# Optimization experiments

Measured on AMD Instinct MI355X. Metric: run time of the kernel, lower is better.

The kernel has to match this reference:

```python
import jax, jax.numpy as jnp
import numpy as np

NEG = -10000.0
MAX_SPAN_LEN = 30
TOP_LAMBDA = 0.4
NUM_CATS = 7
FFNN = 1024
HID = 1024
B, S = 2, 2048
MAX_K = int(S * TOP_LAMBDA)  # 819; static top-k size (input_masks are full)


def fc(x, W, b, g, beta):
    # FullyConnectedLayer: Linear -> GELU(exact) -> LayerNorm (dropout = identity in eval)
    h = jax.nn.gelu(x @ W.T + b, approximate=False)
    mu = jnp.mean(h, axis=-1, keepdims=True)
    var = jnp.var(h, axis=-1, keepdims=True)
    return (h - mu) / jnp.sqrt(var + 1e-5) * g + beta


def setup_inputs():
    key = jax.random.key(0)
    ks = iter(jax.random.split(key, 48))
    def rn(shape, scale=0.02):
        return jax.random.normal(next(ks), shape, jnp.float32) * scale
    NF = NUM_CATS * FFNN
    inp = {
        'input_emb': jax.random.normal(next(ks), (B, S, HID), jnp.float32),
        'input_masks': jnp.ones((B, S), jnp.int32),
        # start/end mention MLPs
        'sm_W': rn((FFNN, HID)), 'sm_b': jnp.zeros((FFNN,)), 'sm_g': jnp.ones((FFNN,)), 'sm_beta': jnp.zeros((FFNN,)),
        'em_W': rn((FFNN, HID)), 'em_b': jnp.zeros((FFNN,)), 'em_g': jnp.ones((FFNN,)), 'em_beta': jnp.zeros((FFNN,)),
        # mention start/end classifiers (Linear(F,1)) and s2e classifier
        'ms_w': rn((FFNN,)), 'ms_b': jnp.zeros(()),
        'me_w': rn((FFNN,)), 'me_b': jnp.zeros(()),
        's2e_W': rn((FFNN, FFNN)), 's2e_b': jnp.zeros((FFNN,)),
        # coref start/end all-category MLPs (output num_cats*ffnn)
        'cs_W': rn((NF, HID)), 'cs_b': jnp.zeros((NF,)), 'cs_g': jnp.ones((NF,)), 'cs_beta': jnp.zeros((NF,)),
        'ce_W': rn((NF, HID)), 'ce_b': jnp.zeros((NF,)), 'ce_g': jnp.ones((NF,)), 'ce_beta': jnp.zeros((NF,)),
        # per-category bilinear antecedent weights/biases
        'Ws2s': rn((NUM_CATS, FFNN, FFNN)), 'We2e': rn((NUM_CATS, FFNN, FFNN)),
        'Ws2e': rn((NUM_CATS, FFNN, FFNN)), 'We2s': rn((NUM_CATS, FFNN, FFNN)),
        'Bs2s': rn((NUM_CATS, FFNN)), 'Be2e': rn((NUM_CATS, FFNN)),
        'Bs2e': rn((NUM_CATS, FFNN)), 'Be2s': rn((NUM_CATS, FFNN)),
    }
    return inp


def reference(input_emb, input_masks, sm_W, sm_b, sm_g, sm_beta, em_W, em_b, em_g, em_beta,
              ms_w, ms_b, me_w, me_b, s2e_W, s2e_b, cs_W, cs_b, cs_g, cs_beta,
              ce_W, ce_b, ce_g, ce_beta, Ws2s, We2e, Ws2e, We2s, Bs2s, Be2e, Bs2e, Be2s):
    # --- mention scores ---
    s = fc(input_emb, sm_W, sm_b, sm_g, sm_beta)   # [B,S,F]
    e = fc(input_emb, em_W, em_b, em_g, em_beta)   # [B,S,F]
    sm = s @ ms_w + ms_b                            # [B,S]
    em = e @ me_w + me_b                            # [B,S]
    joint = jnp.einsum('bsf,btf->bst', s @ s2e_W.T + s2e_b, e)
    scores = joint + sm[:, :, None] + em[:, None, :]
    i = jnp.arange(S)
    band = ((i[None, :] >= i[:, None]) & (i[None, :] - i[:, None] < MAX_SPAN_LEN)).astype(scores.dtype)
    scores = scores + (1.0 - band) * NEG            # mask_tensor (additive)
    # --- top-k span pruning ---
    flat = scores.reshape(B, S * S)
    _, idx = jax.lax.top_k(flat, MAX_K)
    k = (jnp.sum(input_masks, axis=-1).astype(jnp.float32) * TOP_LAMBDA).astype(jnp.int32)
    span_mask = (jnp.arange(MAX_K)[None, :] < k[:, None]).astype(jnp.int32)  # [B,K]
    idx = idx * span_mask + (1 - span_mask) * (S * S - 1)
    idx = jnp.sort(idx, axis=-1)
    start_ids = idx // S
    end_ids = idx % S
    topk_scores = jnp.take_along_axis(flat, idx, axis=1)          # [B,K]
    pair_scores = topk_scores[:, :, None] + topk_scores[:, None, :]
    # --- per-category coref reps (gather then MLP) ---
    start_reps = jnp.take_along_axis(input_emb, start_ids[:, :, None], axis=1)  # [B,K,H]
    end_reps = jnp.take_along_axis(input_emb, end_ids[:, :, None], axis=1)
    a_s = fc(start_reps, cs_W, cs_b, cs_g, cs_beta).reshape(B, MAX_K, NUM_CATS, FFNN).transpose(0, 2, 1, 3)
    a_e = fc(end_reps, ce_W, ce_b, ce_g, ce_beta).reshape(B, MAX_K, NUM_CATS, FFNN).transpose(0, 2, 1, 3)
    # --- per-category bilinear antecedent scores ---
    def bil(x, W, y):
        return jnp.einsum('bnkf,nfg,bnlg->bnkl', x, W, y)
    logits = bil(a_s, Ws2s, a_s) + bil(a_e, We2e, a_e) + bil(a_s, Ws2e, a_e) + bil(a_e, We2s, a_s)
    biases = (jnp.einsum('bnkf,nf->bnk', a_s, Bs2s) + jnp.einsum('bnkf,nf->bnk', a_e, Be2e)
              + jnp.einsum('bnkf,nf->bnk', a_e, Bs2e) + jnp.einsum('bnkf,nf->bnk', a_s, Be2s))[:, :, None, :]
    coref = logits + biases                                        # [B,N,K,K]
    kk = jnp.arange(MAX_K)
    tril = (kk[None, :] < kk[:, None]).astype(coref.dtype)         # strictly-lower (diag=-1)
    mask = tril[None, None] * span_mask[:, None, None, :].astype(coref.dtype)
    coref = coref + (1.0 - mask) * NEG
    return coref + pair_scores[:, None]
```

## Files before the change

### kernel.cpp

```cpp
#include <hip/hip_runtime.h>
#include <hip/hip_bf16.h>
#include <math.h>

#define S_    2048
#define NC_   7
#define MAXK  819
#define NK    1024
#define KP    896
#define Z_    14
#define NEGV  (-10000.0f)

typedef __attribute__((ext_vector_type(8))) short bf16x8;
typedef __attribute__((ext_vector_type(4))) float f32x4;

#define CFENCE asm volatile("" ::: "memory")
#define BAR    do { CFENCE; __builtin_amdgcn_s_barrier(); CFENCE; } while (0)

__device__ __forceinline__ void gload_lds16(const void* g, void* l) {
  __builtin_amdgcn_global_load_lds((const __attribute__((address_space(1))) unsigned int*)g,
                                   (__attribute__((address_space(3))) unsigned int*)l, 16, 0, 0);
}

__device__ __forceinline__ float gelu_exact(float x) {
  return 0.5f * x * (1.0f + erff(x * 0.70710678118654752f));
}
__device__ __forceinline__ unsigned short f2bf(float x) {
  __hip_bfloat16 h = __float2bfloat16(x);
  return *(unsigned short*)&h;
}
__device__ __forceinline__ float bf2f(unsigned short u) {
  __hip_bfloat16 h; *(unsigned short*)&h = u;
  return __bfloat162float(h);
}
__device__ __forceinline__ unsigned fkey(float f) {
  unsigned u = __float_as_uint(f);
  return (u & 0x80000000u) ? ~u : (u | 0x80000000u);
}

template<bool OBF16, int EPI>
__global__ __launch_bounds__(512, 2) void k_gemm8(
    const __hip_bfloat16* __restrict__ A, const __hip_bfloat16* __restrict__ B,
    void* __restrict__ Cv, const float* __restrict__ bias1, const float* __restrict__ bias2,
    const float* __restrict__ tkv, const int* __restrict__ kvp,
    int K, int nbn, long strideA, long strideB, int bmod7, long strideC,
    int ldc, int Mstore, int Nstore)
{
  __shared__ __align__(16) char lds[2][65536];
  const int tid = threadIdx.x;
  const int z = blockIdx.z;
  const int nwg = gridDim.x;
  const int xcd = blockIdx.x & 7, loc = blockIdx.x >> 3;
  const int q = nwg >> 3, r = nwg & 7;
  const int wg = (xcd < r ? xcd * (q + 1) : r * (q + 1) + (xcd - r) * q) + loc;
  const int bm = wg / nbn, bn = wg % nbn;
  const int m0 = bm * 256, n0 = bn * 256;
  const __hip_bfloat16* pA = A + (long)z * strideA;
  const __hip_bfloat16* pB = B + (long)(bmod7 ? (z % 7) : z) * strideB;
  const int wave = tid >> 6, lane = tid & 63;
  const int wm = wave >> 2, wn = wave & 3;
  const int lr = lane & 15, kh = lane >> 4;
  const long Kb = (long)K * 2;

  f32x4 acc[8][4];
  #pragma unroll
  for (int i = 0; i < 8; ++i)
    #pragma unroll
    for (int j = 0; j < 4; ++j)
      #pragma unroll
      for (int rr = 0; rr < 4; ++rr) acc[i][j][rr] = 0.0f;

  auto stageHalf = [&](int bb, int isB, int rh, int kt) {
    const long kbyte = (long)kt * 128;
    const char* basep = isB ? (const char*)pB + (long)(n0 + rh * 128) * Kb
                            : (const char*)pA + (long)(m0 + rh * 128) * Kb;
    #pragma unroll
    for (int j = 0; j < 2; ++j) {
      int off = j * 8192 + tid * 16;
      int row = off >> 7, col = off & 127;
      int gc = col ^ (((rh * 128 + row) & 7) << 4);
      gload_lds16(basep + (long)row * Kb + kbyte + gc,
                  &lds[bb][isB * 32768 + (rh * 128 + row) * 128 + col]);
    }
  };
  auto readA = [&](int c, int g, int kk) -> bf16x8 {
    int row = wm * 128 + g * 16 + lr;
    int colb = kk * 64 + kh * 16;
    return *(const bf16x8*)&lds[c][row * 128 + (colb ^ ((row & 7) << 4))];
  };
  auto readB = [&](int c, int ni, int kk) -> bf16x8 {
    int row = wn * 64 + ni * 16 + lr;
    int colb = kk * 64 + kh * 16;
    return *(const bf16x8*)&lds[c][32768 + row * 128 + (colb ^ ((row & 7) << 4))];
  };
  auto mfma4 = [&](int g0, bf16x8* af, bf16x8* bfr) {
    __builtin_amdgcn_s_setprio(1);
    #pragma unroll
    for (int mi = 0; mi < 4; ++mi)
      #pragma unroll
      for (int ni = 0; ni < 4; ++ni)
        acc[g0 + mi][ni] = __builtin_amdgcn_mfma_f32_16x16x32_bf16(af[mi], bfr[ni], acc[g0 + mi][ni], 0, 0, 0);
    __builtin_amdgcn_s_setprio(0);
  };

  const int nt = K >> 6;
  stageHalf(0, 1, 0, 0);
  stageHalf(0, 1, 1, 0);
  stageHalf(0, 0, 0, 0);
  stageHalf(0, 0, 1, 0);
  if (nt > 1) { stageHalf(1, 1, 0, 1); asm volatile("s_waitcnt vmcnt(2)" ::: "memory"); }
  else        { asm volatile("s_waitcnt vmcnt(0)" ::: "memory"); }
  BAR;

  bf16x8 bfr[4], a0f[4], a1f[4];
  for (int t = 0; t < nt; ++t) {
    const int c = t & 1, cn = c ^ 1;
    #pragma unroll
    for (int i = 0; i < 4; ++i) bfr[i] = readB(c, i, 0);
    #pragma unroll
    for (int i = 0; i < 4; ++i) a0f[i] = readA(c, i, 0);
    if (t + 1 < nt) stageHalf(cn, 1, 1, t + 1);
    BAR;
    mfma4(0, a0f, bfr);
    BAR;
    #pragma unroll
    for (int i = 0; i < 4; ++i) a1f[i] = readA(c, 4 + i, 0);
    if (t + 1 < nt) stageHalf(cn, 0, 0, t + 1);
    BAR;
    mfma4(4, a1f, bfr);
    BAR;
    #pragma unroll
    for (int i = 0; i < 4; ++i) bfr[i] = readB(c, i, 1);
    #pragma unroll
    for (int i = 0; i < 4; ++i) a0f[i] = readA(c, i, 1);
    if (t + 1 < nt) stageHalf(cn, 0, 1, t + 1);
    BAR;
    mfma4(0, a0f, bfr);
    BAR;
    #pragma unroll
    for (int i = 0; i < 4; ++i) a1f[i] = readA(c, 4 + i, 1);
    if (t + 2 < nt) { stageHalf(c, 1, 0, t + 2); asm volatile("s_waitcnt vmcnt(2)" ::: "memory"); }
    else            { asm volatile("s_waitcnt vmcnt(0)" ::: "memory"); }
    BAR;
    mfma4(4, a1f, bfr);
    BAR;
  }

  const long coff = (long)z * strideC;
  int kval = 0, bb_ = 0;
  if (EPI == 2) { bb_ = z / NC_; kval = kvp[bb_]; }
  #pragma unroll
  for (int mi = 0; mi < 8; ++mi) {
    #pragma unroll
    for (int ni = 0; ni < 4; ++ni) {
      int n = n0 + wn * 64 + ni * 16 + lr;
      if (n >= Nstore) continue;
      float badd = 0.f;
      if (EPI == 0) { if (bias1) badd = bias1[n]; }
      if (EPI == 1) badd = (n >= 1024) ? bias2[n - 1024] : bias1[n];
      if (EPI == 2) badd = bias1[z * NK + n] + tkv[bb_ * NK + n];
      #pragma unroll
      for (int rr = 0; rr < 4; ++rr) {
        int m = m0 + wm * 128 + mi * 16 + kh * 4 + rr;
        if (m >= Mstore) continue;
        float v = acc[mi][ni][rr] + badd;
        if (EPI == 2) {
          v += tkv[bb_ * NK + m];
          if (!(n < m && n < kval)) v += NEGV;
        }
        if (OBF16) ((__hip_bfloat16*)Cv)[coff + (long)m * ldc + n] = __float2bfloat16(v);
        else       ((float*)Cv)[coff + (long)m * ldc + n] = v;
      }
    }
  }
}

template<int EPI, int BN>
__global__ __launch_bounds__(512, 1) void k_gemm44(
    const __hip_bfloat16* __restrict__ A, const __hip_bfloat16* __restrict__ B,
    float* __restrict__ Cv, const float* __restrict__ bias1, const float* __restrict__ bias2,
    int K, int nbn, int ldc, int Mstore, int Nstore)
{
  constexpr int NI = BN / 64;
  constexpr int NBH = BN / 128;
  __shared__ __align__(16) char lds[3][16384 + BN * 128];
  const int tid = threadIdx.x;
  const int nwg = gridDim.x;
  const int xcd = blockIdx.x & 7, loc = blockIdx.x >> 3;
  const int q = nwg >> 3, r = nwg & 7;
  const int wg = (xcd < r ? xcd * (q + 1) : r * (q + 1) + (xcd - r) * q) + loc;
  const int bm = wg / nbn, bn = wg % nbn;
  const int m0 = bm * 128, n0 = bn * BN;
  const int wave = tid >> 6, lane = tid & 63;
  const int wm = wave >> 2, wn = wave & 3;
  const int lr = lane & 15, kh = lane >> 4;
  const long Kb = (long)K * 2;

  f32x4 acc[4][NI];
  #pragma unroll
  for (int i = 0; i < 4; ++i)
    #pragma unroll
    for (int j = 0; j < NI; ++j)
      #pragma unroll
      for (int rr = 0; rr < 4; ++rr) acc[i][j][rr] = 0.0f;

  auto stageA = [&](int bb, int kt) {
    const long kbyte = (long)kt * 128;
    const char* basep = (const char*)A + (long)m0 * Kb;
    #pragma unroll
    for (int j = 0; j < 2; ++j) {
      int off = j * 8192 + tid * 16;
      int row = off >> 7, col = off & 127;
      int gc = col ^ ((row & 7) << 4);
      gload_lds16(basep + (long)row * Kb + kbyte + gc, &lds[bb][row * 128 + col]);
    }
  };
  auto stageB = [&](int bb, int kt, int rh) {
    const long kbyte = (long)kt * 128;
    const char* basep = (const char*)B + (long)(n0 + rh * 128) * Kb;
    #pragma unroll
    for (int j = 0; j < 2; ++j) {
      int off = j * 8192 + tid * 16;
      int row = off >> 7, col = off & 127;
      int gc = col ^ (((rh * 128 + row) & 7) << 4);
      gload_lds16(basep + (long)row * Kb + kbyte + gc,
                  &lds[bb][16384 + (rh * 128 + row) * 128 + col]);
    }
  };
  auto readA = [&](int c, int g, int kk) -> bf16x8 {
    int row = wm * 64 + g * 16 + lr;
    int colb = kk * 64 + kh * 16;
    return *(const bf16x8*)&lds[c][row * 128 + (colb ^ ((row & 7) << 4))];
  };
  auto readB = [&](int c, int ni, int kk) -> bf16x8 {
    int row = wn * (NI * 16) + ni * 16 + lr;
    int colb = kk * 64 + kh * 16;
    return *(const bf16x8*)&lds[c][16384 + row * 128 + (colb ^ ((row & 7) << 4))];
  };
  auto mfmaAll = [&](bf16x8* af, bf16x8* bfr) {
    __builtin_amdgcn_s_setprio(1);
    #pragma unroll
    for (int mi = 0; mi < 4; ++mi)
      #pragma unroll
      for (int ni = 0; ni < NI; ++ni)
        acc[mi][ni] = __builtin_amdgcn_mfma_f32_16x16x32_bf16(af[mi], bfr[ni], acc[mi][ni], 0, 0, 0);
    __builtin_amdgcn_s_setprio(0);
  };

  const int nt = K >> 6;
  stageA(0, 0);
  #pragma unroll
  for (int rh = 0; rh < NBH; ++rh) stageB(0, 0, rh);
  if (nt > 1) {
    stageA(1, 1);
    #pragma unroll
    for (int rh = 0; rh < NBH; ++rh) stageB(1, 1, rh);
    if (BN == 256) asm volatile("s_waitcnt vmcnt(6)" ::: "memory");
    else           asm volatile("s_waitcnt vmcnt(4)" ::: "memory");
  } else {
    asm volatile("s_waitcnt vmcnt(0)" ::: "memory");
  }
  BAR;

  bf16x8 af[4], bfr[NI];
  int ct = 0;
  for (int t = 0; t < nt; ++t) {
    const int b2 = (ct + 2 >= 3) ? ct - 1 : ct + 2;
    #pragma unroll
    for (int i = 0; i < NI; ++i) bfr[i] = readB(ct, i, 0);
    #pragma unroll
    for (int i = 0; i < 4; ++i) af[i] = readA(ct, i, 0);
    if (t + 2 < nt) stageA(b2, t + 2);
    BAR;
    mfmaAll(af, bfr);
    BAR;
    #pragma unroll
    for (int i = 0; i < NI; ++i) bfr[i] = readB(ct, i, 1);
    #pragma unroll
    for (int i = 0; i < 4; ++i) af[i] = readA(ct, i, 1);
    if (t + 2 < nt) {
      #pragma unroll
      for (int rh = 0; rh < NBH; ++rh) stageB(b2, t + 2, rh);
      if (BN == 256) asm volatile("s_waitcnt vmcnt(6)" ::: "memory");
      else           asm volatile("s_waitcnt vmcnt(4)" ::: "memory");
    } else {
      asm volatile("s_waitcnt vmcnt(0)" ::: "memory");
    }
    BAR;
    mfmaAll(af, bfr);
    BAR;
    ct = (ct + 1 >= 3) ? 0 : ct + 1;
  }

  #pragma unroll
  for (int mi = 0; mi < 4; ++mi) {
    #pragma unroll
    for (int ni = 0; ni < NI; ++ni) {
      int n = n0 + wn * (NI * 16) + ni * 16 + lr;
      if (n >= Nstore) continue;
      float badd = 0.f;
      if (EPI == 0) { if (bias1) badd = bias1[n]; }
      if (EPI == 1) badd = (n >= 1024) ? bias2[n - 1024] : bias1[n];
      #pragma unroll
      for (int rr = 0; rr < 4; ++rr) {
        int m = m0 + wm * 64 + mi * 16 + kh * 4 + rr;
        if (m >= Mstore) continue;
        Cv[(long)m * ldc + n] = acc[mi][ni][rr] + badd;
      }
    }
  }
}

template<bool APAT>
__global__ __launch_bounds__(256) void k_packsplit3(const float* __restrict__ s1, long stride1,
                                                    const float* __restrict__ s2, int split,
                                                    __hip_bfloat16* __restrict__ dst) {
  long idx4 = ((long)blockIdx.x * 256 + threadIdx.x) * 4;
  int rrow = (int)(idx4 >> 10), c = (int)(idx4 & 1023);
  const float* src = (rrow < split) ? s1 + (long)rrow * stride1 + c
                                    : s2 + (long)(rrow - split) * 1024 + c;
  float4 v = *(const float4*)src;
  float f[4] = {v.x, v.y, v.z, v.w};
  unsigned short h[4], l4[4];
  #pragma unroll
  for (int i = 0; i < 4; ++i) {
    h[i] = f2bf(f[i]);
    l4[i] = f2bf(f[i] - bf2f(h[i]));
  }
  unsigned short* d = (unsigned short*)dst + (long)rrow * 3072;
  ushort4 hv = {h[0], h[1], h[2], h[3]};
  ushort4 lv = {l4[0], l4[1], l4[2], l4[3]};
  *(ushort4*)(d + c)        = hv;
  *(ushort4*)(d + 1024 + c) = APAT ? hv : lv;
  *(ushort4*)(d + 2048 + c) = APAT ? lv : hv;
}

__global__ __launch_bounds__(256) void k_cast4(const float* __restrict__ x,
                                               __hip_bfloat16* __restrict__ y, long n4) {
  long i = (long)blockIdx.x * 256 + threadIdx.x;
  if (i >= n4) return;
  float4 v = ((const float4*)x)[i];
  ushort4 o = {f2bf(v.x), f2bf(v.y), f2bf(v.z), f2bf(v.w)};
  ((ushort4*)y)[i] = o;
}

__global__ __launch_bounds__(256) void k_packBbig(const float* __restrict__ Ws2s,
                                                  const float* __restrict__ We2e,
                                                  const float* __restrict__ Ws2e,
                                                  const float* __restrict__ We2s,
                                                  __hip_bfloat16* __restrict__ dst) {
  long idx4 = ((long)blockIdx.x * 256 + threadIdx.x) * 4;
  long rowid = idx4 >> 11;
  int c = (int)(idx4 & 2047);
  int cat = (int)(rowid >> 11);
  int n = (int)(rowid & 2047);
  const float* src;
  if (n < 1024) src = (c < 1024) ? Ws2s + ((long)cat * 1024 + n) * 1024 + c
                                 : Ws2e + ((long)cat * 1024 + n) * 1024 + (c - 1024);
  else          src = (c < 1024) ? We2s + ((long)cat * 1024 + (n - 1024)) * 1024 + c
                                 : We2e + ((long)cat * 1024 + (n - 1024)) * 1024 + (c - 1024);
  float4 v = *(const float4*)src;
  ushort4 o = {f2bf(v.x), f2bf(v.y), f2bf(v.z), f2bf(v.w)};
  *(ushort4*)((unsigned short*)dst + idx4) = o;
}

__global__ __launch_bounds__(512) void k_ln_se(float* __restrict__ se,
                                               const float* __restrict__ sg, const float* __restrict__ sbe,
                                               const float* __restrict__ eg, const float* __restrict__ ebe,
                                               const float* __restrict__ msw, const float* __restrict__ msb,
                                               const float* __restrict__ mew, const float* __restrict__ meb,
                                               float* __restrict__ smv, float* __restrict__ emv,
                                               __hip_bfloat16* __restrict__ ssp) {
  int r = blockIdx.x;
  int tid = threadIdx.x;
  int half = tid >> 8;
  int c4 = tid & 255;
  int w8 = tid >> 6;
  const float* g    = half ? eg : sg;
  const float* beta = half ? ebe : sbe;
  const float* wv   = half ? mew : msw;
  float4* rowp = (float4*)(se + (long)r * 2048 + half * 1024);
  float4 x = rowp[c4];
  float v[4] = {gelu_exact(x.x), gelu_exact(x.y), gelu_exact(x.z), gelu_exact(x.w)};
  float s = v[0] + v[1] + v[2] + v[3];
  float s2 = v[0]*v[0] + v[1]*v[1] + v[2]*v[2] + v[3]*v[3];
  __shared__ float red0[8], red1[8];
  for (int off = 32; off; off >>= 1) { s += __shfl_xor(s, off); s2 += __shfl_xor(s2, off); }
  if ((tid & 63) == 0) { red0[w8] = s; red1[w8] = s2; }
  __syncthreads();
  s  = red0[half*4] + red0[half*4+1] + red0[half*4+2] + red0[half*4+3];
  s2 = red1[half*4] + red1[half*4+1] + red1[half*4+2] + red1[half*4+3];
  float mu  = s / 1024.0f;
  float var = s2 / 1024.0f - mu * mu;
  float inv = 1.0f / sqrtf(var + 1e-5f);
  float4 gg = ((const float4*)g)[c4], bb = ((const float4*)beta)[c4];
  float y[4] = {(v[0]-mu)*inv*gg.x + bb.x, (v[1]-mu)*inv*gg.y + bb.y,
                (v[2]-mu)*inv*gg.z + bb.z, (v[3]-mu)*inv*gg.w + bb.w};
  float4 w4 = ((const float4*)wv)[c4];
  float d = y[0]*w4.x + y[1]*w4.y + y[2]*w4.z + y[3]*w4.w;
  for (int off = 32; off; off >>= 1) d += __shfl_xor(d, off);
  __syncthreads();
  if ((tid & 63) == 0) red0[w8] = d;
  __syncthreads();
  if ((tid & 255) == 0) {
    float dv = red0[half*4] + red0[half*4+1] + red0[half*4+2] + red0[half*4+3];
    if (half == 0) smv[r] = dv + msb[0];
    else           emv[r] = dv + meb[0];
  }
  if (half == 0) {
    unsigned short h[4], l4[4];
    #pragma unroll
    for (int i = 0; i < 4; ++i) { h[i] = f2bf(y[i]); l4[i] = f2bf(y[i] - bf2f(h[i])); }
    ushort4 hv = {h[0], h[1], h[2], h[3]};
    ushort4 lv = {l4[0], l4[1], l4[2], l4[3]};
    unsigned short* dst = (unsigned short*)ssp + (long)r * 3072 + c4 * 4;
    *(ushort4*)dst          = hv;
    *(ushort4*)(dst + 1024) = hv;
    *(ushort4*)(dst + 2048) = lv;
  } else {
    float4 yo = {y[0], y[1], y[2], y[3]};
    rowp[c4] = yo;
  }
}

__global__ __launch_bounds__(256) void k_gelu_ln_cats(const __hip_bfloat16* __restrict__ h,
                                                      const float* __restrict__ g,
                                                      const float* __restrict__ beta,
                                                      __hip_bfloat16* __restrict__ a_cat, int half) {
  int r = blockIdx.x;
  int b = (r >= KP) ? 1 : 0, k = r - KP * b;
  const ushort4* row = (const ushort4*)((const unsigned short*)h + (long)r * 7168);
  float v[28];
  float s = 0.f, s2 = 0.f;
  #pragma unroll
  for (int j = 0; j < 7; ++j) {
    ushort4 u = row[threadIdx.x + 256 * j];
    #pragma unroll
    for (int e = 0; e < 4; ++e) {
      float x = bf2f(((const unsigned short*)&u)[e]);
      float ge = gelu_exact(x);
      v[j * 4 + e] = ge; s += ge; s2 += ge * ge;
    }
  }
  __shared__ float red0[4], red1[4];
  for (int off = 32; off; off >>= 1) { s += __shfl_xor(s, off); s2 += __shfl_xor(s2, off); }
  int w = threadIdx.x >> 6;
  if ((threadIdx.x & 63) == 0) { red0[w] = s; red1[w] = s2; }
  __syncthreads();
  s  = red0[0] + red0[1] + red0[2] + red0[3];
  s2 = red1[0] + red1[1] + red1[2] + red1[3];
  float mu  = s / 7168.0f;
  float var = s2 / 7168.0f - mu * mu;
  float inv = 1.0f / sqrtf(var + 1e-5f);
  #pragma unroll
  for (int j = 0; j < 7; ++j) {
    int c0 = (threadIdx.x + 256 * j) * 4;
    int n = c0 >> 10, f = c0 & 1023;
    unsigned short o[4];
    #pragma unroll
    for (int e = 0; e < 4; ++e)
      o[e] = f2bf((v[j * 4 + e] - mu) * inv * g[c0 + e] + beta[c0 + e]);
    ushort4 ov = {o[0], o[1], o[2], o[3]};
    *(ushort4*)((unsigned short*)a_cat + ((long)((b * NC_ + n) * NK + k)) * 2048 + half * 1024 + f) = ov;
  }
}

__global__ __launch_bounds__(512) void k_band(const float* __restrict__ s2m,
                                              const float* __restrict__ se,
                                              const float* __restrict__ smv,
                                              const float* __restrict__ emv,
                                              float* __restrict__ band) {
  __shared__ float ebuf[2][1024];
  int blk = blockIdx.x;
  int b = blk >> 8;
  int s0 = (blk & 255) * 8;
  int w = threadIdx.x >> 6, l = threadIdx.x & 63;
  int s = s0 + w;
  int tid = threadIdx.x;
  float sreg[16];
  const float* sp = s2m + ((long)(b << 11) + s) * 1024;
  #pragma unroll
  for (int qq = 0; qq < 16; ++qq) sreg[qq] = sp[l + 64 * qq];
  float myS = smv[(b << 11) + s];
  if (l < 32) {
    int j = l;
    if (j >= 30 || s + j >= S_)
      band[((long)(b << 11) + s) * 32 + j] = -3.0e38f;
  }
  {
    const float* ep = se + ((long)(b << 11) + s0) * 2048 + 1024;
    ebuf[0][tid * 2]     = ep[tid * 2];
    ebuf[0][tid * 2 + 1] = ep[tid * 2 + 1];
  }
  for (int it = 0; it < 37; ++it) {
    int t = s0 + it;
    __syncthreads();
    if (it + 1 < 37 && s0 + it + 1 < S_) {
      const float* ep = se + ((long)(b << 11) + s0 + it + 1) * 2048 + 1024;
      ebuf[(it + 1) & 1][tid * 2]     = ep[tid * 2];
      ebuf[(it + 1) & 1][tid * 2 + 1] = ep[tid * 2 + 1];
    }
    int j = t - s;
    if (t < S_ && j >= 0 && j < 30) {
      const float* eb = ebuf[it & 1];
      float acc = 0.f;
      #pragma unroll
      for (int qq = 0; qq < 16; ++qq) acc += sreg[qq] * eb[l + 64 * qq];
      for (int off = 32; off; off >>= 1) acc += __shfl_xor(acc, off);
      if (l == 0)
        band[((long)(b << 11) + s) * 32 + j] = acc + myS + emv[(b << 11) + t];
    }
  }
}

__global__ __launch_bounds__(1024) void k_tkzero(unsigned* __restrict__ ghist,
                                                 unsigned* __restrict__ gcnt) {
  int i = blockIdx.x * 1024 + threadIdx.x;
  if (i < 2 * 4096) ghist[i] = 0;
  if (i < 2) gcnt[i] = 0;
}

__global__ __launch_bounds__(1024) void k_tkhist(const float* __restrict__ band,
                                                 unsigned* __restrict__ ghist) {
  int b = blockIdx.y;
  const float* bb = band + (long)b * 65536;
  __shared__ unsigned lh[4096];
  int tid = threadIdx.x;
  #pragma unroll
  for (int j = 0; j < 4; ++j) lh[tid + j * 1024] = 0;
  __syncthreads();
  int base = blockIdx.x * 4096;
  #pragma unroll
  for (int j = 0; j < 4; ++j) {
    unsigned key = fkey(bb[base + tid + j * 1024]);
    atomicAdd(&lh[key >> 20], 1u);
  }
  __syncthreads();
  #pragma unroll
  for (int j = 0; j < 4; ++j) {
    unsigned v = lh[tid + j * 1024];
    if (v) atomicAdd(&ghist[b * 4096 + tid + j * 1024], v);
  }
}

__global__ __launch_bounds__(1024) void k_tkscan(const unsigned* __restrict__ ghist,
                                                 const int* __restrict__ masks,
                                                 unsigned* __restrict__ sel) {
  int b = blockIdx.x;
  int tid = threadIdx.x;
  __shared__ unsigned cs[1024];
  __shared__ int red[16];
  __shared__ int sh_kv;
  int pm = masks[b * S_ + tid] + masks[b * S_ + 1024 + tid];
  for (int off = 32; off; off >>= 1) pm += __shfl_xor(pm, off);
  if ((tid & 63) == 0) red[tid >> 6] = pm;
  __syncthreads();
  if (tid == 0) {
    int msum = 0;
    for (int i = 0; i < 16; ++i) msum += red[i];
    int kv = (int)((float)msum * 0.4f);
    if (kv > MAXK) kv = MAXK;
    sh_kv = kv;
  }
  __syncthreads();
  int kv = sh_kv;
  unsigned hbin[4];
  unsigned ssum = 0;
  #pragma unroll
  for (int j = 0; j < 4; ++j) { hbin[j] = ghist[b * 4096 + tid * 4 + j]; ssum += hbin[j]; }
  cs[tid] = ssum;
  __syncthreads();
  for (int off = 1; off < 1024; off <<= 1) {
    unsigned add = (tid + off < 1024) ? cs[tid + off] : 0u;
    __syncthreads();
    cs[tid] += add;
    __syncthreads();
  }
  unsigned above = cs[tid] - ssum;
  if (kv > 0) {
    unsigned aa = above;
    for (int j = 3; j >= 0; --j) {
      if (aa < (unsigned)kv && aa + hbin[j] >= (unsigned)kv) sel[b * 2] = (unsigned)(tid * 4 + j);
      aa += hbin[j];
    }
  }
  if (tid == 0) {
    sel[b * 2 + 1] = (unsigned)kv;
    if (kv == 0) sel[b * 2] = 0xFFFFFFFFu;
  }
}

__global__ __launch_bounds__(1024) void k_tkcollect(const float* __restrict__ band,
                                                    const unsigned* __restrict__ sel,
                                                    unsigned* __restrict__ cand,
                                                    unsigned* __restrict__ gcnt) {
  int b = blockIdx.y;
  const float* bb = band + (long)b * 65536;
  unsigned thr = sel[b * 2];
  int base = blockIdx.x * 4096;
  int tid = threadIdx.x;
  #pragma unroll
  for (int j = 0; j < 4; ++j) {
    int i = base + tid + j * 1024;
    unsigned key = fkey(bb[i]);
    if ((key >> 20) >= thr) {
      unsigned p = atomicAdd(&gcnt[b], 1u);
      cand[(long)b * 65536 + p] = (unsigned)i;
    }
  }
}

__device__ __forceinline__ void bitonic1024(unsigned* buf) {
  int tid = threadIdx.x;
  __syncthreads();
  for (int k = 2; k <= 1024; k <<= 1)
    for (int j = k >> 1; j > 0; j >>= 1) {
      int ixj = tid ^ j;
      if (ixj > tid) {
        unsigned a = buf[tid], c = buf[ixj];
        bool up = ((tid & k) == 0);
        if (up ? (a > c) : (a < c)) { buf[tid] = c; buf[ixj] = a; }
      }
      __syncthreads();
    }
}

__global__ __launch_bounds__(1024) void k_tkfinal(const float* __restrict__ band,
                                                  const unsigned* __restrict__ cand,
                                                  const unsigned* __restrict__ gcnt,
                                                  const unsigned* __restrict__ sel,
                                                  int* __restrict__ starts, int* __restrict__ ends,
                                                  float* __restrict__ tk, int* __restrict__ kvalid_out) {
  int b = blockIdx.x;
  const float* bb = band + (long)b * 65536;
  const unsigned* cd = cand + (long)b * 65536;
  int nC = (int)gcnt[b];
  int kv = (int)sel[b * 2 + 1];
  __shared__ unsigned hist[256];
  __shared__ int sh_digit, sh_R;
  __shared__ unsigned cntG, cntE;
  __shared__ unsigned listG[832];
  __shared__ unsigned listE[1024];
  __shared__ unsigned buf[1024];
  int tid = threadIdx.x;

  unsigned prefix = 0;
  int R = kv;
  if (kv > 0) {
    for (int shift = 24; shift >= 0; shift -= 8) {
      if (tid < 256) hist[tid] = 0;
      __syncthreads();
      for (int j = tid; j < nC; j += 1024) {
        unsigned key = fkey(bb[cd[j]]);
        bool ok = (shift == 24) || ((key >> (shift + 8)) == (prefix >> (shift + 8)));
        if (ok) atomicAdd(&hist[(key >> shift) & 255u], 1u);
      }
      __syncthreads();
      if (tid == 0) {
        unsigned cum = 0; int d;
        for (d = 255; d >= 0; --d) {
          unsigned hc = hist[d];
          if (cum + hc >= (unsigned)R) break;
          cum += hc;
        }
        if (d < 0) d = 0;
        sh_digit = d; sh_R = R - (int)cum;
      }
      __syncthreads();
      prefix |= ((unsigned)sh_digit) << shift;
      R = sh_R;
      __syncthreads();
    }
  }
  if (tid == 0) { cntG = 0; cntE = 0; }
  __syncthreads();
  if (kv > 0) {
    for (int j = tid; j < nC; j += 1024) {
      unsigned i = cd[j];
      unsigned key = fkey(bb[i]);
      if (key > prefix) { unsigned p = atomicAdd(&cntG, 1u); if (p < 832) listG[p] = i; }
      else if (key == prefix) { unsigned p = atomicAdd(&cntE, 1u); if (p < 1024) listE[p] = i; }
    }
  }
  __syncthreads();
  int nG = (int)cntG, nE = (int)cntE, need = R;
  buf[tid] = (tid < nE) ? listE[tid] : 0xFFFFFFFFu;
  bitonic1024(buf);
  if (tid < need) listG[nG + tid] = buf[tid];
  __syncthreads();
  unsigned v2 = (tid < (unsigned)kv) ? listG[tid] : 0xFFFFFFFFu;
  __syncthreads();
  buf[tid] = v2;
  bitonic1024(buf);
  {
    int s, t; float val;
    if (tid < kv) {
      unsigned i = buf[tid];
      s = (int)(i >> 5); t = s + (int)(i & 31);
      val = bb[i];
    } else {
      s = S_ - 1; t = S_ - 1;
      val = bb[(S_ - 1) * 32 + 0];
    }
    starts[b * NK + tid] = s;
    ends[b * NK + tid] = t;
    tk[b * NK + tid] = val;
  }
  if (tid == 0) kvalid_out[b] = kv;
}

__global__ __launch_bounds__(256) void k_gather(const float* __restrict__ emb,
                                                const int* __restrict__ starts,
                                                const int* __restrict__ ends,
                                                __hip_bfloat16* __restrict__ reps_s,
                                                __hip_bfloat16* __restrict__ reps_e) {
  int r = blockIdx.x;
  int b = (r >= KP) ? 1 : 0, k = r - KP * b;
  long ob = (long)r * 1024;
  const float4* ps = (const float4*)(emb + ((long)b * S_ + starts[b * NK + k]) * 1024);
  const float4* pe = (const float4*)(emb + ((long)b * S_ + ends[b * NK + k]) * 1024);
  unsigned short* ds = (unsigned short*)reps_s + ob;
  unsigned short* de = (unsigned short*)reps_e + ob;
  int c4 = threadIdx.x;
  float4 a = ps[c4], e = pe[c4];
  ushort4 oa = {f2bf(a.x), f2bf(a.y), f2bf(a.z), f2bf(a.w)};
  ushort4 oe = {f2bf(e.x), f2bf(e.y), f2bf(e.z), f2bf(e.w)};
  *(ushort4*)(ds + c4 * 4) = oa;
  *(ushort4*)(de + c4 * 4) = oe;
}

__global__ __launch_bounds__(256) void k_bias(const __hip_bfloat16* __restrict__ a_cat,
                                              const float* __restrict__ Bs2s, const float* __restrict__ Be2e,
                                              const float* __restrict__ Bs2e, const float* __restrict__ Be2s,
                                              float* __restrict__ biasv) {
  int w = threadIdx.x >> 6, l = threadIdx.x & 63;
  int rid = blockIdx.x * 4 + w;
  if (rid >= Z_ * KP) return;
  int z = rid / KP, li = rid - z * KP;
  int cat = z % NC_;
  const unsigned short* ar = (const unsigned short*)a_cat + ((long)z * NK + li) * 2048;
  const float* b1 = Bs2s + cat * 1024;
  const float* b2 = Be2s + cat * 1024;
  const float* b3 = Be2e + cat * 1024;
  const float* b4 = Bs2e + cat * 1024;
  float acc = 0.f;
  for (int qq = 0; qq < 16; ++qq) {
    int c = l + 64 * qq;
    acc += bf2f(ar[c]) * (b1[c] + b2[c]);
    acc += bf2f(ar[1024 + c]) * (b3[c] + b4[c]);
  }
  for (int off = 32; off; off >>= 1) acc += __shfl_xor(acc, off);
  if (l == 0) biasv[z * NK + li] = acc;
}

extern "C" void kernel_launch(void* const* d_in, const int* in_sizes, int n_in,
                              void* d_out, int out_size, void* d_ws, size_t ws_size,
                              hipStream_t stream) {
  const float* x_emb = (const float*)d_in[0];
  const int*   masks = (const int*)d_in[1];
  const float* smW  = (const float*)d_in[2];
  const float* smb  = (const float*)d_in[3];
  const float* smg  = (const float*)d_in[4];
  const float* smbe = (const float*)d_in[5];
  const float* emW  = (const float*)d_in[6];
  const float* embb = (const float*)d_in[7];
  const float* emg  = (const float*)d_in[8];
  const float* embe = (const float*)d_in[9];
  const float* msw  = (const float*)d_in[10];
  const float* msb  = (const float*)d_in[11];
  const float* mew  = (const float*)d_in[12];
  const float* meb  = (const float*)d_in[13];
  const float* s2eW = (const float*)d_in[14];
  const float* s2eb = (const float*)d_in[15];
  const float* csW  = (const float*)d_in[16];
  const float* csb  = (const float*)d_in[17];
  const float* csg  = (const float*)d_in[18];
  const float* csbe = (const float*)d_in[19];
  const float* ceW  = (const float*)d_in[20];
  const float* ceb  = (const float*)d_in[21];
  const float* ceg  = (const float*)d_in[22];
  const float* cebe = (const float*)d_in[23];
  const float* Ws2s = (const float*)d_in[24];
  const float* We2e = (const float*)d_in[25];
  const float* Ws2e = (const float*)d_in[26];
  const float* We2s = (const float*)d_in[27];
  const float* Bs2s = (const float*)d_in[28];
  const float* Be2e = (const float*)d_in[29];
  const float* Bs2e = (const float*)d_in[30];
  const float* Be2s = (const float*)d_in[31];
  float* outp = (float*)d_out;
  char* ws = (char*)d_ws;
  (void)in_sizes; (void)n_in; (void)out_size; (void)ws_size;

  const size_t o_embsp = 0;
  const size_t o_bse   = 25165824;
  const size_t o_ssp   = 0;
  const size_t o_s2W   = 25165824;
  const size_t o_repss = 0;
  const size_t o_repse = 4194304;
  const size_t o_csWb  = 8388608;
  const size_t o_ceWb  = 23068672;
  const size_t o_Bbig  = 0;
  const size_t o_se    = 37748736;
  const size_t o_s2    = 71303168;
  const size_t o_h     = 88080384;
  const size_t o_acat  = 146800640;
  const size_t o_smv   = 205520896;
  const size_t o_emv   = o_smv + 16384;
  const size_t o_band  = o_emv + 16384;
  const size_t o_starts= o_band + 524288;
  const size_t o_ends  = o_starts + 8192;
  const size_t o_tk    = o_ends + 8192;
  const size_t o_kv    = o_tk + 8192;
  const size_t o_biasv = o_kv + 256;
  const size_t o_ghist = o_biasv + 61440;
  const size_t o_sel   = o_ghist + 32768;
  const size_t o_gcnt  = o_sel + 256;
  const size_t o_cand  = o_gcnt + 256;

  __hip_bfloat16* embsp = (__hip_bfloat16*)(ws + o_embsp);
  __hip_bfloat16* bse   = (__hip_bfloat16*)(ws + o_bse);
  __hip_bfloat16* ssp   = (__hip_bfloat16*)(ws + o_ssp);
  __hip_bfloat16* s2Wsp = (__hip_bfloat16*)(ws + o_s2W);
  __hip_bfloat16* repss = (__hip_bfloat16*)(ws + o_repss);
  __hip_bfloat16* repse = (__hip_bfloat16*)(ws + o_repse);
  __hip_bfloat16* csWb  = (__hip_bfloat16*)(ws + o_csWb);
  __hip_bfloat16* ceWb  = (__hip_bfloat16*)(ws + o_ceWb);
  __hip_bfloat16* Bbig  = (__hip_bfloat16*)(ws + o_Bbig);
  float* se_buf = (float*)(ws + o_se);
  float* s2_buf = (float*)(ws + o_s2);
  __hip_bfloat16* h_buf = (__hip_bfloat16*)(ws + o_h);
  __hip_bfloat16* Vcat  = (__hip_bfloat16*)(ws + o_h);
  __hip_bfloat16* a_cat = (__hip_bfloat16*)(ws + o_acat);
  float* smv_p = (float*)(ws + o_smv);
  float* emv_p = (float*)(ws + o_emv);
  float* band_p = (float*)(ws + o_band);
  int* starts_p = (int*)(ws + o_starts);
  int* ends_p = (int*)(ws + o_ends);
  float* tk_p = (float*)(ws + o_tk);
  int* kv_p = (int*)(ws + o_kv);
  float* biasv_p = (float*)(ws + o_biasv);
  unsigned* ghist_p = (unsigned*)(ws + o_ghist);
  unsigned* sel_p = (unsigned*)(ws + o_sel);
  unsigned* gcnt_p = (unsigned*)(ws + o_gcnt);
  unsigned* cand_p = (unsigned*)(ws + o_cand);

  k_packsplit3<true ><<<4096, 256, 0, stream>>>(x_emb, 1024, x_emb, 4096, embsp);
  k_packsplit3<false><<<2048, 256, 0, stream>>>(smW, 1024, emW, 1024, bse);
  k_gemm44<1, 256><<<dim3(256, 1, 1), 512, 0, stream>>>(embsp, bse, se_buf, smb, embb,
      3072, 8, 2048, 4096, 2048);
  k_ln_se<<<4096, 512, 0, stream>>>(se_buf, smg, smbe, emg, embe, msw, msb, mew, meb,
                                    smv_p, emv_p, ssp);

  k_packsplit3<false><<<1024, 256, 0, stream>>>(s2eW, 1024, s2eW, 1024, s2Wsp);
  k_gemm44<0, 128><<<dim3(256, 1, 1), 512, 0, stream>>>(ssp, s2Wsp, s2_buf, s2eb, nullptr,
      3072, 8, 1024, 4096, 1024);
  k_band<<<512, 512, 0, stream>>>(s2_buf, se_buf, smv_p, emv_p, band_p);

  k_tkzero<<<9, 1024, 0, stream>>>(ghist_p, gcnt_p);
  k_tkhist<<<dim3(16, 2), 1024, 0, stream>>>(band_p, ghist_p);
  k_tkscan<<<2, 1024, 0, stream>>>(ghist_p, masks, sel_p);
  k_tkcollect<<<dim3(16, 2), 1024, 0, stream>>>(band_p, sel_p, cand_p, gcnt_p);
  k_tkfinal<<<2, 1024, 0, stream>>>(band_p, cand_p, gcnt_p, sel_p,
                                    starts_p, ends_p, tk_p, kv_p);

  k_gather<<<2 * KP, 256, 0, stream>>>(x_emb, starts_p, ends_p, repss, repse);
  k_cast4<<<7168, 256, 0, stream>>>(csW, csWb, 1835008);
  k_cast4<<<7168, 256, 0, stream>>>(ceW, ceWb, 1835008);
  k_gemm8<true, 0><<<dim3(196, 1, 1), 512, 0, stream>>>(repss, csWb, h_buf, csb, nullptr,
      nullptr, nullptr, 1024, 28, 0, 0, 0, 0, 7168, 2 * KP, 7168);
  k_gelu_ln_cats<<<2 * KP, 256, 0, stream>>>(h_buf, csg, csbe, a_cat, 0);
  k_gemm8<true, 0><<<dim3(196, 1, 1), 512, 0, stream>>>(repse, ceWb, h_buf, ceb, nullptr,
      nullptr, nullptr, 1024, 28, 0, 0, 0, 0, 7168, 2 * KP, 7168);
  k_packBbig<<<28672, 256, 0, stream>>>(Ws2s, We2e, Ws2e, We2s, Bbig);
  k_gelu_ln_cats<<<2 * KP, 256, 0, stream>>>(h_buf, ceg, cebe, a_cat, 1);

  k_gemm8<true, 0><<<dim3(32, 1, Z_), 512, 0, stream>>>(a_cat, Bbig, Vcat, nullptr, nullptr,
      nullptr, nullptr, 2048, 8, (long)NK * 2048, (long)2048 * 2048, 1, (long)NK * 2048, 2048, NK, 2048);
  k_bias<<<(Z_ * KP) / 4, 256, 0, stream>>>(a_cat, Bs2s, Be2e, Bs2e, Be2s, biasv_p);
  k_gemm8<false, 2><<<dim3(16, 1, Z_), 512, 0, stream>>>(a_cat, Vcat, outp, biasv_p, nullptr,
      tk_p, kv_p, 2048, 4, (long)NK * 2048, (long)NK * 2048, 0, (long)MAXK * MAXK, MAXK, MAXK, MAXK);
}
```

Baseline: 684.1 us.

## Replace large-tile GEMMs with 128x128 tiles, merge start/end coref GEMMs

Swaps the 128xBN triple-buffered GEMM and the 256x256 coref projection GEMMs for a new 128x128 double-buffered kernel with higher occupancy (launch bounds 4), so small-M GEMMs fill more workgroups across the GPU. The start and end coref MLP GEMMs become one launch that picks the operand and bias sets by row, and their weight casts and gelu-layernorm passes are merged the same way. The histogram zeroing kernel becomes a memset. The cost is a simpler 2-stage pipeline with less data reuse per tile, plus a larger intermediate h buffer holding both halves at once.

```diff
diff --git a/kernel.cpp b/kernel.cpp
--- a/kernel.cpp
+++ b/kernel.cpp
@@ -50,8 +50,8 @@
   const int z = blockIdx.z;
   const int nwg = gridDim.x;
   const int xcd = blockIdx.x & 7, loc = blockIdx.x >> 3;
-  const int q = nwg >> 3, r = nwg & 7;
-  const int wg = (xcd < r ? xcd * (q + 1) : r * (q + 1) + (xcd - r) * q) + loc;
+  const int q = nwg >> 3, rr = nwg & 7;
+  const int wg = (xcd < rr ? xcd * (q + 1) : rr * (q + 1) + (xcd - rr) * q) + loc;
   const int bm = wg / nbn, bn = wg % nbn;
   const int m0 = bm * 256, n0 = bn * 256;
   const __hip_bfloat16* pA = A + (long)z * strideA;
@@ -67,7 +67,7 @@
     #pragma unroll
     for (int j = 0; j < 4; ++j)
       #pragma unroll
-      for (int rr = 0; rr < 4; ++rr) acc[i][j][rr] = 0.0f;
+      for (int r4 = 0; r4 < 4; ++r4) acc[i][j][r4] = 0.0f;
 
   auto stageHalf = [&](int bb, int isB, int rh, int kt) {
     const long kbyte = (long)kt * 128;
@@ -156,13 +156,12 @@
       if (n >= Nstore) continue;
       float badd = 0.f;
       if (EPI == 0) { if (bias1) badd = bias1[n]; }
-      if (EPI == 1) badd = (n >= 1024) ? bias2[n - 1024] : bias1[n];
       if (EPI == 2) badd = bias1[z * NK + n] + tkv[bb_ * NK + n];
       #pragma unroll
-      for (int rr = 0; rr < 4; ++rr) {
-        int m = m0 + wm * 128 + mi * 16 + kh * 4 + rr;
+      for (int r4 = 0; r4 < 4; ++r4) {
+        int m = m0 + wm * 128 + mi * 16 + kh * 4 + r4;
         if (m >= Mstore) continue;
-        float v = acc[mi][ni][rr] + badd;
+        float v = acc[mi][ni][r4] + badd;
         if (EPI == 2) {
           v += tkv[bb_ * NK + m];
           if (!(n < m && n < kval)) v += NEGV;
@@ -174,56 +173,54 @@
   }
 }
 
-template<int EPI, int BN>
-__global__ __launch_bounds__(512, 1) void k_gemm44(
-    const __hip_bfloat16* __restrict__ A, const __hip_bfloat16* __restrict__ B,
-    float* __restrict__ Cv, const float* __restrict__ bias1, const float* __restrict__ bias2,
-    int K, int nbn, int ldc, int Mstore, int Nstore)
+template<bool OBF16, int EPI, bool FCM>
+__global__ __launch_bounds__(512, 4) void k_gemm2b(
+    const __hip_bfloat16* __restrict__ A, const __hip_bfloat16* __restrict__ A2,
+    const __hip_bfloat16* __restrict__ B, const __hip_bfloat16* __restrict__ B2,
+    void* __restrict__ Cv, const float* __restrict__ bias1, const float* __restrict__ bias2,
+    int K, int nbn, int ldc, int Mstore, int Nstore, int Msplit)
 {
-  constexpr int NI = BN / 64;
-  constexpr int NBH = BN / 128;
-  __shared__ __align__(16) char lds[3][16384 + BN * 128];
+  __shared__ __align__(16) char lds[2][32768];
   const int tid = threadIdx.x;
   const int nwg = gridDim.x;
   const int xcd = blockIdx.x & 7, loc = blockIdx.x >> 3;
-  const int q = nwg >> 3, r = nwg & 7;
-  const int wg = (xcd < r ? xcd * (q + 1) : r * (q + 1) + (xcd - r) * q) + loc;
+  const int q = nwg >> 3, rr = nwg & 7;
+  const int wg = (xcd < rr ? xcd * (q + 1) : rr * (q + 1) + (xcd - rr) * q) + loc;
   const int bm = wg / nbn, bn = wg % nbn;
-  const int m0 = bm * 128, n0 = bn * BN;
+  const int m0 = bm * 128, n0 = bn * 128;
+  const long Kb = (long)K * 2;
+  bool set1 = FCM && (m0 >= Msplit);
+  const __hip_bfloat16* pA = set1 ? (A2 - (long)Msplit * K) : A;
+  const __hip_bfloat16* pB = set1 ? B2 : B;
   const int wave = tid >> 6, lane = tid & 63;
   const int wm = wave >> 2, wn = wave & 3;
   const int lr = lane & 15, kh = lane >> 4;
-  const long Kb = (long)K * 2;
-
-  f32x4 acc[4][NI];
+
+  f32x4 acc[4][2];
   #pragma unroll
   for (int i = 0; i < 4; ++i)
     #pragma unroll
-    for (int j = 0; j < NI; ++j)
+    for (int j = 0; j < 2; ++j)
       #pragma unroll
-      for (int rr = 0; rr < 4; ++rr) acc[i][j][rr] = 0.0f;
-
-  auto stageA = [&](int bb, int kt) {
+      for (int r4 = 0; r4 < 4; ++r4) acc[i][j][r4] = 0.0f;
+
+  auto stage = [&](int bb, int kt) {
     const long kbyte = (long)kt * 128;
-    const char* basep = (const char*)A + (long)m0 * Kb;
+    const char* bA = (const char*)pA + (long)m0 * Kb;
+    const char* bB = (const char*)pB + (long)n0 * Kb;
     #pragma unroll
     for (int j = 0; j < 2; ++j) {
       int off = j * 8192 + tid * 16;
       int row = off >> 7, col = off & 127;
       int gc = col ^ ((row & 7) << 4);
-      gload_lds16(basep + (long)row * Kb + kbyte + gc, &lds[bb][row * 128 + col]);
-    }
-  };
-  auto stageB = [&](int bb, int kt, int rh) {
-    const long kbyte = (long)kt * 128;
-    const char* basep = (const char*)B + (long)(n0 + rh * 128) * Kb;
+      gload_lds16(bA + (long)row * Kb + kbyte + gc, &lds[bb][row * 128 + col]);
+    }
     #pragma unroll
     for (int j = 0; j < 2; ++j) {
       int off = j * 8192 + tid * 16;
       int row = off >> 7, col = off & 127;
-      int gc = col ^ (((rh * 128 + row) & 7) << 4);
-      gload_lds16(basep + (long)row * Kb + kbyte + gc,
-                  &lds[bb][16384 + (rh * 128 + row) * 128 + col]);
+      int gc = col ^ ((row & 7) << 4);
+      gload_lds16(bB + (long)row * Kb + kbyte + gc, &lds[bb][16384 + row * 128 + col]);
     }
   };
   auto readA = [&](int c, int g, int kk) -> bf16x8 {
@@ -232,79 +229,55 @@
     return *(const bf16x8*)&lds[c][row * 128 + (colb ^ ((row & 7) << 4))];
   };
   auto readB = [&](int c, int ni, int kk) -> bf16x8 {
-    int row = wn * (NI * 16) + ni * 16 + lr;
+    int row = wn * 32 + ni * 16 + lr;
     int colb = kk * 64 + kh * 16;
     return *(const bf16x8*)&lds[c][16384 + row * 128 + (colb ^ ((row & 7) << 4))];
   };
-  auto mfmaAll = [&](bf16x8* af, bf16x8* bfr) {
-    __builtin_amdgcn_s_setprio(1);
-    #pragma unroll
-    for (int mi = 0; mi < 4; ++mi)
+
+  const int nt = K >> 6;
+  stage(0, 0);
+  asm volatile("s_waitcnt vmcnt(0)" ::: "memory");
+  BAR;
+
+  for (int t = 0; t < nt; ++t) {
+    const int c = t & 1, cn = c ^ 1;
+    if (t + 1 < nt) stage(cn, t + 1);
+    bf16x8 af[4], bfr[2];
+    #pragma unroll
+    for (int kk = 0; kk < 2; ++kk) {
       #pragma unroll
-      for (int ni = 0; ni < NI; ++ni)
-        acc[mi][ni] = __builtin_amdgcn_mfma_f32_16x16x32_bf16(af[mi], bfr[ni], acc[mi][ni], 0, 0, 0);
-    __builtin_amdgcn_s_setprio(0);
-  };
-
-  const int nt = K >> 6;
-  stageA(0, 0);
-  #pragma unroll
-  for (int rh = 0; rh < NBH; ++rh) stageB(0, 0, rh);
-  if (nt > 1) {
-    stageA(1, 1);
-    #pragma unroll
-    for (int rh = 0; rh < NBH; ++rh) stageB(1, 1, rh);
-    if (BN == 256) asm volatile("s_waitcnt vmcnt(6)" ::: "memory");
-    else           asm volatile("s_waitcnt vmcnt(4)" ::: "memory");
-  } else {
+      for (int i = 0; i < 4; ++i) af[i] = readA(c, i, kk);
+      #pragma unroll
+      for (int i = 0; i < 2; ++i) bfr[i] = readB(c, i, kk);
+      __builtin_amdgcn_s_setprio(1);
+      #pragma unroll
+      for (int mi = 0; mi < 4; ++mi)
+        #pragma unroll
+        for (int ni = 0; ni < 2; ++ni)
+          acc[mi][ni] = __builtin_amdgcn_mfma_f32_16x16x32_bf16(af[mi], bfr[ni], acc[mi][ni], 0, 0, 0);
+      __builtin_amdgcn_s_setprio(0);
+    }
     asm volatile("s_waitcnt vmcnt(0)" ::: "memory");
-  }
-  BAR;
-
-  bf16x8 af[4], bfr[NI];
-  int ct = 0;
-  for (int t = 0; t < nt; ++t) {
-    const int b2 = (ct + 2 >= 3) ? ct - 1 : ct + 2;
-    #pragma unroll
-    for (int i = 0; i < NI; ++i) bfr[i] = readB(ct, i, 0);
-    #pragma unroll
-    for (int i = 0; i < 4; ++i) af[i] = readA(ct, i, 0);
-    if (t + 2 < nt) stageA(b2, t + 2);
     BAR;
-    mfmaAll(af, bfr);
-    BAR;
-    #pragma unroll
-    for (int i = 0; i < NI; ++i) bfr[i] = readB(ct, i, 1);
-    #pragma unroll
-    for (int i = 0; i < 4; ++i) af[i] = readA(ct, i, 1);
-    if (t + 2 < nt) {
-      #pragma unroll
-      for (int rh = 0; rh < NBH; ++rh) stageB(b2, t + 2, rh);
-      if (BN == 256) asm volatile("s_waitcnt vmcnt(6)" ::: "memory");
-      else           asm volatile("s_waitcnt vmcnt(4)" ::: "memory");
-    } else {
-      asm volatile("s_waitcnt vmcnt(0)" ::: "memory");
-    }
-    BAR;
-    mfmaAll(af, bfr);
-    BAR;
-    ct = (ct + 1 >= 3) ? 0 : ct + 1;
-  }
-
+  }
+
+  const float* bp1 = (FCM && set1) ? bias2 : bias1;
   #pragma unroll
   for (int mi = 0; mi < 4; ++mi) {
     #pragma unroll
-    for (int ni = 0; ni < NI; ++ni) {
-      int n = n0 + wn * (NI * 16) + ni * 16 + lr;
+    for (int ni = 0; ni < 2; ++ni) {
+      int n = n0 + wn * 32 + ni * 16 + lr;
       if (n >= Nstore) continue;
       float badd = 0.f;
-      if (EPI == 0) { if (bias1) badd = bias1[n]; }
+      if (EPI == 0) { if (bp1) badd = bp1[n]; }
       if (EPI == 1) badd = (n >= 1024) ? bias2[n - 1024] : bias1[n];
       #pragma unroll
-      for (int rr = 0; rr < 4; ++rr) {
-        int m = m0 + wm * 64 + mi * 16 + kh * 4 + rr;
+      for (int r4 = 0; r4 < 4; ++r4) {
+        int m = m0 + wm * 64 + mi * 16 + kh * 4 + r4;
         if (m >= Mstore) continue;
-        Cv[(long)m * ldc + n] = acc[mi][ni][rr] + badd;
+        float v = acc[mi][ni][r4] + badd;
+        if (OBF16) ((__hip_bfloat16*)Cv)[(long)m * ldc + n] = __float2bfloat16(v);
+        else       ((float*)Cv)[(long)m * ldc + n] = v;
       }
     }
   }
@@ -334,10 +307,14 @@
   *(ushort4*)(d + 2048 + c) = APAT ? lv : hv;
 }
 
-__global__ __launch_bounds__(256) void k_cast4(const float* __restrict__ x,
-                                               __hip_bfloat16* __restrict__ y, long n4) {
+__global__ __launch_bounds__(256) void k_cast4d(const float* __restrict__ x0,
+                                                __hip_bfloat16* __restrict__ y0,
+                                                const float* __restrict__ x1,
+                                                __hip_bfloat16* __restrict__ y1, long n4) {
   long i = (long)blockIdx.x * 256 + threadIdx.x;
   if (i >= n4) return;
+  const float* x = blockIdx.y ? x1 : x0;
+  __hip_bfloat16* y = blockIdx.y ? y1 : y0;
   float4 v = ((const float4*)x)[i];
   ushort4 o = {f2bf(v.x), f2bf(v.y), f2bf(v.z), f2bf(v.w)};
   ((ushort4*)y)[i] = o;
@@ -423,11 +400,17 @@
 }
 
 __global__ __launch_bounds__(256) void k_gelu_ln_cats(const __hip_bfloat16* __restrict__ h,
-                                                      const float* __restrict__ g,
-                                                      const float* __restrict__ beta,
-                                                      __hip_bfloat16* __restrict__ a_cat, int half) {
+                                                      const float* __restrict__ sg,
+                                                      const float* __restrict__ sbe,
+                                                      const float* __restrict__ eg,
+                                                      const float* __restrict__ ebe,
+                                                      __hip_bfloat16* __restrict__ a_cat) {
   int r = blockIdx.x;
-  int b = (r >= KP) ? 1 : 0, k = r - KP * b;
+  int half = (r >= 2 * KP) ? 1 : 0;
+  int r2 = r - half * 2 * KP;
+  int b = (r2 >= KP) ? 1 : 0, k = r2 - KP * b;
+  const float* g    = half ? eg : sg;
+  const float* beta = half ? ebe : sbe;
   const ushort4* row = (const ushort4*)((const unsigned short*)h + (long)r * 7168);
   float v[28];
   float s = 0.f, s2 = 0.f;
@@ -510,13 +493,6 @@
         band[((long)(b << 11) + s) * 32 + j] = acc + myS + emv[(b << 11) + t];
     }
   }
-}
-
-__global__ __launch_bounds__(1024) void k_tkzero(unsigned* __restrict__ ghist,
-                                                 unsigned* __restrict__ gcnt) {
-  int i = blockIdx.x * 1024 + threadIdx.x;
-  if (i < 2 * 4096) ghist[i] = 0;
-  if (i < 2) gcnt[i] = 0;
 }
 
 __global__ __launch_bounds__(1024) void k_tkhist(const float* __restrict__ band,
@@ -813,9 +789,9 @@
   const size_t o_kv    = o_tk + 8192;
   const size_t o_biasv = o_kv + 256;
   const size_t o_ghist = o_biasv + 61440;
-  const size_t o_sel   = o_ghist + 32768;
-  const size_t o_gcnt  = o_sel + 256;
-  const size_t o_cand  = o_gcnt + 256;
+  const size_t o_gcnt  = o_ghist + 32768;
+  const size_t o_sel   = o_gcnt + 256;
+  const size_t o_cand  = o_sel + 256;
 
   __hip_bfloat16* embsp = (__hip_bfloat16*)(ws + o_embsp);
   __hip_bfloat16* bse   = (__hip_bfloat16*)(ws + o_bse);
@@ -828,7 +804,7 @@
   __hip_bfloat16* Bbig  = (__hip_bfloat16*)(ws + o_Bbig);
   float* se_buf = (float*)(ws + o_se);
   float* s2_buf = (float*)(ws + o_s2);
-  __hip_bfloat16* h_buf = (__hip_bfloat16*)(ws + o_h);
+  __hip_bfloat16* h_all = (__hip_bfloat16*)(ws + o_h);
   __hip_bfloat16* Vcat  = (__hip_bfloat16*)(ws + o_h);
   __hip_bfloat16* a_cat = (__hip_bfloat16*)(ws + o_acat);
   float* smv_p = (float*)(ws + o_smv);
@@ -840,23 +816,23 @@
   int* kv_p = (int*)(ws + o_kv);
   float* biasv_p = (float*)(ws + o_biasv);
   unsigned* ghist_p = (unsigned*)(ws + o_ghist);
+  unsigned* gcnt_p = (unsigned*)(ws + o_gcnt);
   unsigned* sel_p = (unsigned*)(ws + o_sel);
-  unsigned* gcnt_p = (unsigned*)(ws + o_gcnt);
   unsigned* cand_p = (unsigned*)(ws + o_cand);
 
   k_packsplit3<true ><<<4096, 256, 0, stream>>>(x_emb, 1024, x_emb, 4096, embsp);
   k_packsplit3<false><<<2048, 256, 0, stream>>>(smW, 1024, emW, 1024, bse);
-  k_gemm44<1, 256><<<dim3(256, 1, 1), 512, 0, stream>>>(embsp, bse, se_buf, smb, embb,
-      3072, 8, 2048, 4096, 2048);
+  k_gemm2b<false, 1, false><<<512, 512, 0, stream>>>(embsp, nullptr, bse, nullptr,
+      se_buf, smb, embb, 3072, 16, 2048, 4096, 2048, 0);
   k_ln_se<<<4096, 512, 0, stream>>>(se_buf, smg, smbe, emg, embe, msw, msb, mew, meb,
                                     smv_p, emv_p, ssp);
 
   k_packsplit3<false><<<1024, 256, 0, stream>>>(s2eW, 1024, s2eW, 1024, s2Wsp);
-  k_gemm44<0, 128><<<dim3(256, 1, 1), 512, 0, stream>>>(ssp, s2Wsp, s2_buf, s2eb, nullptr,
-      3072, 8, 1024, 4096, 1024);
+  k_gemm2b<false, 0, false><<<256, 512, 0, stream>>>(ssp, nullptr, s2Wsp, nullptr,
+      s2_buf, s2eb, nullptr, 3072, 8, 1024, 4096, 1024, 0);
   k_band<<<512, 512, 0, stream>>>(s2_buf, se_buf, smv_p, emv_p, band_p);
 
-  k_tkzero<<<9, 1024, 0, stream>>>(ghist_p, gcnt_p);
+  hipMemsetAsync(ws + o_ghist, 0, 33024, stream);
   k_tkhist<<<dim3(16, 2), 1024, 0, stream>>>(band_p, ghist_p);
   k_tkscan<<<2, 1024, 0, stream>>>(ghist_p, masks, sel_p);
   k_tkcollect<<<dim3(16, 2), 1024, 0, stream>>>(band_p, sel_p, cand_p, gcnt_p);
@@ -864,15 +840,11 @@
                                     starts_p, ends_p, tk_p, kv_p);
 
   k_gather<<<2 * KP, 256, 0, stream>>>(x_emb, starts_p, ends_p, repss, repse);
-  k_cast4<<<7168, 256, 0, stream>>>(csW, csWb, 1835008);
-  k_cast4<<<7168, 256, 0, stream>>>(ceW, ceWb, 1835008);
-  k_gemm8<true, 0><<<dim3(196, 1, 1), 512, 0, stream>>>(repss, csWb, h_buf, csb, nullptr,
-      nullptr, nullptr, 1024, 28, 0, 0, 0, 0, 7168, 2 * KP, 7168);
-  k_gelu_ln_cats<<<2 * KP, 256, 0, stream>>>(h_buf, csg, csbe, a_cat, 0);
-  k_gemm8<true, 0><<<dim3(196, 1, 1), 512, 0, stream>>>(repse, ceWb, h_buf, ceb, nullptr,
-      nullptr, nullptr, 1024, 28, 0, 0, 0, 0, 7168, 2 * KP, 7168);
+  k_cast4d<<<dim3(7168, 2), 256, 0, stream>>>(csW, csWb, ceW, ceWb, 1835008);
+  k_gemm2b<true, 0, true><<<1568, 512, 0, stream>>>(repss, repse, csWb, ceWb,
+      h_all, csb, ceb, 1024, 56, 7168, 3584, 7168, 2 * KP);
   k_packBbig<<<28672, 256, 0, stream>>>(Ws2s, We2e, Ws2e, We2s, Bbig);
-  k_gelu_ln_cats<<<2 * KP, 256, 0, stream>>>(h_buf, ceg, cebe, a_cat, 1);
+  k_gelu_ln_cats<<<3584, 256, 0, stream>>>(h_all, csg, csbe, ceg, cebe, a_cat);
 
   k_gemm8<true, 0><<<dim3(32, 1, Z_), 512, 0, stream>>>(a_cat, Bbig, Vcat, nullptr, nullptr,
       nullptr, nullptr, 2048, 8, (long)NK * 2048, (long)2048 * 2048, 1, (long)NK * 2048, 2048, NK, 2048);
```

Result: no change. 684.6 us (+0.1%).
